# Kernel optimization log

Hardware: AMD Instinct MI355X
Metric: run time of the kernel (lower is better)

Reference implementation:

```python
import jax, jax.numpy as jnp
import numpy as np

B, N, E = 8, 10000, 320000   # graphs per batch, nodes per graph, edges per graph
C_IN, C_OUT = 128, 128
WEIGHT_STDDEV = 0.01


def setup_inputs() -> dict:
    key = jax.random.key(0)
    k_x, k_r, k_c, k_v, k_w = jax.random.split(key, 5)
    x = jax.random.normal(k_x, (B, N, C_IN), dtype=jnp.float32)
    rows = jax.random.randint(k_r, (B, E), 0, N, dtype=jnp.int32)
    cols = jax.random.randint(k_c, (B, E), 0, N, dtype=jnp.int32)
    vals = jax.random.uniform(k_v, (B, E), dtype=jnp.float32)
    W = WEIGHT_STDDEV * jax.random.normal(k_w, (C_IN, C_OUT), dtype=jnp.float32)
    b = jnp.zeros((C_OUT,), dtype=jnp.float32)  # bias_constant = 0.0
    return {"x": x, "rows": rows, "cols": cols, "vals": vals, "W": W, "b": b}


def reference(x, rows, cols, vals, W, b):
    # Per-graph sparse adjacency matmul: (A_i @ x_i), A_i in COO form.
    def spmm(r, c, v, xi):
        # gather source node features, weight by edge value, scatter-add to dst rows
        msg = v[:, None] * xi[c]                      # [E, C_IN]
        return jax.ops.segment_sum(msg, r, num_segments=N)  # [N, C_IN]

    ax = jax.vmap(spmm)(rows, cols, vals, x)          # [B, N, C_IN]
    out = jnp.einsum('bnc,co->bno', ax, W) + b        # dense transform + bias
    return jax.nn.relu(out)
```

## Files before the change

kernel.cpp:

```cpp
#include <hip/hip_runtime.h>

constexpr int BGRAPHS = 8;
constexpr int NNODES  = 10000;
constexpr int NEDGES  = 320000;
constexpr int CH      = 128;
constexpr int TOTROWS = BGRAPHS * NNODES;
constexpr int TOTEDGE = BGRAPHS * NEDGES;

constexpr int BROWS  = 32;
constexpr int BPG    = (NNODES + BROWS - 1) / BROWS;
constexpr int TOTB   = BPG * BGRAPHS;
constexpr int CHUNK  = 4000;
constexpr int NCHUNK = TOTEDGE / CHUNK;
constexpr int CAPB   = 1536;

constexpr int XROWS  = 64;
constexpr int XBPG   = (NNODES + XROWS - 1) / XROWS;
constexpr int XGRID  = 8 * XBPG;
constexpr int WTLD   = 136;

using bf16x8 = __attribute__((ext_vector_type(8))) short;
using f32x4  = __attribute__((ext_vector_type(4))) float;

__device__ __forceinline__ unsigned pack_bf16(float a, float b) {
    unsigned ua = __float_as_uint(a);
    unsigned ub = __float_as_uint(b);
    ua = (ua + 0x7FFFu + ((ua >> 16) & 1u)) >> 16;
    ub = (ub + 0x7FFFu + ((ub >> 16) & 1u)) >> 16;
    return ua | (ub << 16);
}
__device__ __forceinline__ ushort bf16_1(float f) {
    unsigned u = __float_as_uint(f);
    u = (u + 0x7FFFu + ((u >> 16) & 1u)) >> 16;
    return (ushort)u;
}

__device__ __forceinline__ unsigned pack_edge(int row5, int gcol, float v) {
    int q = __float2int_rz(v * 1024.0f);
    q = min(q, 1023);
    return ((unsigned)row5 << 27) | ((unsigned)gcol << 10) | (unsigned)q;
}

__global__ __launch_bounds__(256) void zero_int_kernel(int* __restrict__ p, int n) {
    int i = blockIdx.x * blockDim.x + threadIdx.x;
    if (i < n) p[i] = 0;
}

__global__ __launch_bounds__(256) void zero_f4_kernel(float* __restrict__ p, int n4) {
    int i = blockIdx.x * blockDim.x + threadIdx.x;
    int stride = gridDim.x * blockDim.x;
    float4 z = make_float4(0.f, 0.f, 0.f, 0.f);
    for (int j = i; j < n4; j += stride) reinterpret_cast<float4*>(p)[j] = z;
}

constexpr int SMEM_BYTES = 37120;

__global__ __launch_bounds__(256, 4) void prep_kernel(
    const int* __restrict__ rows, const int* __restrict__ cols,
    const float* __restrict__ vals, int* __restrict__ cursor,
    unsigned* __restrict__ edata,
    const float* __restrict__ x, const float* __restrict__ W,
    ushort* __restrict__ xwb) {
    __shared__ __align__(16) char smem[SMEM_BYTES];
    const int tid = threadIdx.x;

    if (blockIdx.x < NCHUNK) {
        unsigned* srec   = reinterpret_cast<unsigned*>(smem);
        unsigned* sdst   = reinterpret_cast<unsigned*>(smem + 16000);
        int*      h      = reinterpret_cast<int*>(smem + 32000);
        int*      lstart = reinterpret_cast<int*>(smem + 33280);
        int*      sbase  = reinterpret_cast<int*>(smem + 34560);
        int*      scur   = reinterpret_cast<int*>(smem + 35840);

        for (int k = tid; k < BPG; k += 256) h[k] = 0;
        __syncthreads();
        const int g  = blockIdx.x & 7;
        const int c  = blockIdx.x >> 3;
        const int e0 = g * NEDGES + c * CHUNK;
        for (int j = e0 + 4 * tid; j < e0 + CHUNK; j += 1024) {
            int4 r4 = *reinterpret_cast<const int4*>(&rows[j]);
            atomicAdd(&h[r4.x >> 5], 1);
            atomicAdd(&h[r4.y >> 5], 1);
            atomicAdd(&h[r4.z >> 5], 1);
            atomicAdd(&h[r4.w >> 5], 1);
        }
        __syncthreads();
        if (tid < 64) {
            const int b0 = tid * 5;
            int v[5];
            int s = 0;
            #pragma unroll
            for (int t = 0; t < 5; ++t) {
                int b = b0 + t;
                v[t] = (b < BPG) ? h[b] : 0;
                s += v[t];
            }
            int inc = s;
            #pragma unroll
            for (int off = 1; off < 64; off <<= 1) {
                int u = __shfl_up(inc, off);
                if (tid >= off) inc += u;
            }
            int excl = inc - s;
            #pragma unroll
            for (int t = 0; t < 5; ++t) {
                int b = b0 + t;
                if (b < BPG) { lstart[b] = excl; excl += v[t]; }
            }
        } else {
            for (int k = tid - 64; k < BPG; k += 192) {
                scur[k] = 0;
                sbase[k] = h[k] ? atomicAdd(&cursor[g * BPG + k], h[k]) : 0;
            }
        }
        __syncthreads();
        const int gbase = g * NNODES;
        for (int j = e0 + 4 * tid; j < e0 + CHUNK; j += 1024) {
            int4   r4 = *reinterpret_cast<const int4*>(&rows[j]);
            int4   c4 = *reinterpret_cast<const int4*>(&cols[j]);
            float4 v4 = *reinterpret_cast<const float4*>(&vals[j]);
            {
                int k = r4.x >> 5;
                int r = atomicAdd(&scur[k], 1);
                int pos = lstart[k] + r;
                int off = sbase[k] + r;
                srec[pos] = pack_edge(r4.x & 31, gbase + c4.x, v4.x);
                sdst[pos] = (off < CAPB) ? (unsigned)(k * CAPB + off) : 0xFFFFFFFFu;
            }
            {
                int k = r4.y >> 5;
                int r = atomicAdd(&scur[k], 1);
                int pos = lstart[k] + r;
                int off = sbase[k] + r;
                srec[pos] = pack_edge(r4.y & 31, gbase + c4.y, v4.y);
                sdst[pos] = (off < CAPB) ? (unsigned)(k * CAPB + off) : 0xFFFFFFFFu;
            }
            {
                int k = r4.z >> 5;
                int r = atomicAdd(&scur[k], 1);
                int pos = lstart[k] + r;
                int off = sbase[k] + r;
                srec[pos] = pack_edge(r4.z & 31, gbase + c4.z, v4.z);
                sdst[pos] = (off < CAPB) ? (unsigned)(k * CAPB + off) : 0xFFFFFFFFu;
            }
            {
                int k = r4.w >> 5;
                int r = atomicAdd(&scur[k], 1);
                int pos = lstart[k] + r;
                int off = sbase[k] + r;
                srec[pos] = pack_edge(r4.w & 31, gbase + c4.w, v4.w);
                sdst[pos] = (off < CAPB) ? (unsigned)(k * CAPB + off) : 0xFFFFFFFFu;
            }
        }
        __syncthreads();
        const size_t gb = (size_t)g * BPG * CAPB;
        for (int i = tid; i < CHUNK; i += 256) {
            unsigned d = sdst[i];
            if (d != 0xFFFFFFFFu) edata[gb + d] = srec[i];
        }
    } else {
        ushort* Wt = reinterpret_cast<ushort*>(smem);

        const int b2  = blockIdx.x - NCHUNK;
        const int g   = b2 & 7;
        const int rb  = b2 >> 3;
        const int row0 = rb * XROWS;
        const int rows_ib = min(XROWS, NNODES - row0);

        const float4* W4 = reinterpret_cast<const float4*>(W);
        for (int i = tid; i < 4096; i += 256) {
            float4 wv = W4[i];
            int k = i >> 5;
            int n = (i & 31) * 4;
            Wt[(n    ) * WTLD + k] = bf16_1(wv.x);
            Wt[(n + 1) * WTLD + k] = bf16_1(wv.y);
            Wt[(n + 2) * WTLD + k] = bf16_1(wv.z);
            Wt[(n + 3) * WTLD + k] = bf16_1(wv.w);
        }
        __syncthreads();

        const int w    = tid >> 6;
        const int lane = tid & 63;
        const int m16  = lane & 15;
        const int G    = lane >> 4;

        const int rA = min(row0 + w * 16 + m16, NNODES - 1);
        const float* xrow = x + ((size_t)g * NNODES + rA) * CH;

        f32x4 acc[8];
        #pragma unroll
        for (int nt = 0; nt < 8; ++nt) acc[nt] = (f32x4){0.f, 0.f, 0.f, 0.f};

        #pragma unroll
        for (int kt = 0; kt < 4; ++kt) {
            const int k0 = kt * 32 + G * 8;
            const float4* ap = reinterpret_cast<const float4*>(xrow + k0);
            float4 p = ap[0];
            float4 q = ap[1];
            union { bf16x8 vec; unsigned u[4]; } af;
            af.u[0] = pack_bf16(p.x, p.y);
            af.u[1] = pack_bf16(p.z, p.w);
            af.u[2] = pack_bf16(q.x, q.y);
            af.u[3] = pack_bf16(q.z, q.w);
            const bf16x8 avec = af.vec;
            #pragma unroll
            for (int nt = 0; nt < 8; ++nt) {
                const bf16x8 bvec = *reinterpret_cast<const bf16x8*>(
                    &Wt[(nt * 16 + m16) * WTLD + k0]);
                acc[nt] = __builtin_amdgcn_mfma_f32_16x16x32_bf16(avec, bvec,
                                                                  acc[nt], 0, 0, 0);
            }
        }

        ushort* og = xwb + ((size_t)g * NNODES + row0) * CH;
        #pragma unroll
        for (int nt = 0; nt < 8; ++nt) {
            const int col = nt * 16 + m16;
            #pragma unroll
            for (int reg = 0; reg < 4; ++reg) {
                const int rloc = w * 16 + G * 4 + reg;
                if (rloc < rows_ib)
                    og[(size_t)rloc * CH + col] = bf16_1(acc[nt][reg]);
            }
        }
    }
}

__global__ __launch_bounds__(512) void bucket_gather_kernel(
    const ushort* __restrict__ xwb, const int* __restrict__ cursor,
    const unsigned* __restrict__ edata, const float* __restrict__ bias,
    float* __restrict__ out) {
    __shared__ unsigned sorted[CAPB];
    __shared__ int cnt[BROWS];
    __shared__ int rstart[BROWS + 1];
    __shared__ int cur[BROWS];

    const int g = blockIdx.x & 7;
    const int k = blockIdx.x >> 3;
    const int bid = g * BPG + k;
    const int tid = threadIdx.x;
    const int w = tid >> 6;
    const int lane = tid & 63;
    const int eh = lane >> 5;
    const int c4 = lane & 31;
    const int rows_ib = min(BROWS, NNODES - k * BROWS);

    const size_t base = (size_t)bid * CAPB;
    const int total = min(cursor[bid], CAPB);

    unsigned e0, e1, e2;
    const bool h0 = tid < total, h1 = tid + 512 < total, h2 = tid + 1024 < total;
    if (h0) e0 = edata[base + tid];
    if (h1) e1 = edata[base + tid + 512];
    if (h2) e2 = edata[base + tid + 1024];

    if (tid < BROWS) cnt[tid] = 0;
    __syncthreads();
    if (h0) atomicAdd(&cnt[e0 >> 27], 1);
    if (h1) atomicAdd(&cnt[e1 >> 27], 1);
    if (h2) atomicAdd(&cnt[e2 >> 27], 1);
    __syncthreads();
    if (w == 0) {
        int v = (lane < BROWS) ? cnt[lane] : 0;
        int s = v;
        #pragma unroll
        for (int off = 1; off < BROWS; off <<= 1) {
            int u = __shfl_up(s, off);
            if (lane >= off) s += u;
        }
        if (lane < BROWS) { rstart[lane + 1] = s; cur[lane] = s - v; }
        if (lane == 0) rstart[0] = 0;
    }
    __syncthreads();
    if (h0) { int p = atomicAdd(&cur[e0 >> 27], 1); sorted[p] = e0; }
    if (h1) { int p = atomicAdd(&cur[e1 >> 27], 1); sorted[p] = e1; }
    if (h2) { int p = atomicAdd(&cur[e2 >> 27], 1); sorted[p] = e2; }
    __syncthreads();

    const char* xwbB = reinterpret_cast<const char*>(xwb);
    const int coff = 8 * c4;

    #define DECODE_V(M) fmaf((float)((M) & 1023u), 1.0f/1024.0f, 1.0f/2048.0f)
    #define DECODE_A(M) (((M) >> 2) & 0x01FFFF00u)

    float4 acc[4];
    #pragma unroll
    for (int i = 0; i < 4; ++i) {
        acc[i] = make_float4(0.f, 0.f, 0.f, 0.f);
        const int row = w + 8 * i;
        if (row < rows_ib) {
            int j    = rstart[row];
            int jend = rstart[row + 1];
            float4 aA = acc[i];
            float4 aB = make_float4(0.f, 0.f, 0.f, 0.f);
            for (; j + 7 < jend; j += 8) {
                unsigned m0 = sorted[j     + eh];
                unsigned m1 = sorted[j + 2 + eh];
                unsigned m2 = sorted[j + 4 + eh];
                unsigned m3 = sorted[j + 6 + eh];
                uint2 u0 = *reinterpret_cast<const uint2*>(xwbB + (DECODE_A(m0) + coff));
                uint2 u1 = *reinterpret_cast<const uint2*>(xwbB + (DECODE_A(m1) + coff));
                uint2 u2 = *reinterpret_cast<const uint2*>(xwbB + (DECODE_A(m2) + coff));
                uint2 u3 = *reinterpret_cast<const uint2*>(xwbB + (DECODE_A(m3) + coff));
                float v0 = DECODE_V(m0);
                float v1 = DECODE_V(m1);
                float v2 = DECODE_V(m2);
                float v3 = DECODE_V(m3);
                aA.x += v0 * __uint_as_float(u0.x << 16);
                aA.y += v0 * __uint_as_float(u0.x & 0xFFFF0000u);
                aA.z += v0 * __uint_as_float(u0.y << 16);
                aA.w += v0 * __uint_as_float(u0.y & 0xFFFF0000u);
                aB.x += v1 * __uint_as_float(u1.x << 16);
                aB.y += v1 * __uint_as_float(u1.x & 0xFFFF0000u);
                aB.z += v1 * __uint_as_float(u1.y << 16);
                aB.w += v1 * __uint_as_float(u1.y & 0xFFFF0000u);
                aA.x += v2 * __uint_as_float(u2.x << 16);
                aA.y += v2 * __uint_as_float(u2.x & 0xFFFF0000u);
                aA.z += v2 * __uint_as_float(u2.y << 16);
                aA.w += v2 * __uint_as_float(u2.y & 0xFFFF0000u);
                aB.x += v3 * __uint_as_float(u3.x << 16);
                aB.y += v3 * __uint_as_float(u3.x & 0xFFFF0000u);
                aB.z += v3 * __uint_as_float(u3.y << 16);
                aB.w += v3 * __uint_as_float(u3.y & 0xFFFF0000u);
            }
            for (; j + 1 < jend; j += 2) {
                unsigned m = sorted[j + eh];
                uint2 u = *reinterpret_cast<const uint2*>(xwbB + (DECODE_A(m) + coff));
                float v = DECODE_V(m);
                aA.x += v * __uint_as_float(u.x << 16);
                aA.y += v * __uint_as_float(u.x & 0xFFFF0000u);
                aA.z += v * __uint_as_float(u.y << 16);
                aA.w += v * __uint_as_float(u.y & 0xFFFF0000u);
            }
            if (j < jend && eh == 0) {
                unsigned m = sorted[j];
                uint2 u = *reinterpret_cast<const uint2*>(xwbB + (DECODE_A(m) + coff));
                float v = DECODE_V(m);
                aA.x += v * __uint_as_float(u.x << 16);
                aA.y += v * __uint_as_float(u.x & 0xFFFF0000u);
                aA.z += v * __uint_as_float(u.y << 16);
                aA.w += v * __uint_as_float(u.y & 0xFFFF0000u);
            }
            acc[i] = make_float4(aA.x + aB.x, aA.y + aB.y,
                                 aA.z + aB.z, aA.w + aB.w);
        }
    }

    const float4 b4 = *reinterpret_cast<const float4*>(&bias[4 * c4]);
    #pragma unroll
    for (int i = 0; i < 4; ++i) {
        const int row = w + 8 * i;
        if (row < rows_ib) {
            float4 a = acc[i];
            a.x += __shfl_down(a.x, 32);
            a.y += __shfl_down(a.y, 32);
            a.z += __shfl_down(a.z, 32);
            a.w += __shfl_down(a.w, 32);
            if (eh == 0) {
                a.x = fmaxf(a.x + b4.x, 0.f);
                a.y = fmaxf(a.y + b4.y, 0.f);
                a.z = fmaxf(a.z + b4.z, 0.f);
                a.w = fmaxf(a.w + b4.w, 0.f);
                *reinterpret_cast<float4*>(
                    &out[((size_t)g * NNODES + (size_t)k * BROWS + row) * CH + 4 * c4]) = a;
            }
        }
    }
}

__global__ __launch_bounds__(256) void transform_kernel(
    float* __restrict__ io, const float* __restrict__ W,
    const float* __restrict__ bias, int totalRows) {
    __shared__ float Ws[CH * CH];
    __shared__ float rbuf[8][CH];
    for (int i = threadIdx.x * 4; i < CH * CH; i += blockDim.x * 4) {
        *reinterpret_cast<float4*>(&Ws[i]) =
            *reinterpret_cast<const float4*>(&W[i]);
    }
    const int rs = threadIdx.x >> 5;
    const int o4 = threadIdx.x & 31;
    const float4 bias4 = *reinterpret_cast<const float4*>(&bias[4 * o4]);
    __syncthreads();
    for (int base = blockIdx.x * 8; base < totalRows; base += gridDim.x * 8) {
        const int row = base + rs;
        *reinterpret_cast<float4*>(&rbuf[rs][4 * o4]) =
            *reinterpret_cast<const float4*>(&io[(size_t)row * CH + 4 * o4]);
        __syncthreads();
        float4 acc = bias4;
        #pragma unroll 8
        for (int c = 0; c < CH; ++c) {
            const float rv = rbuf[rs][c];
            const float4 w4 =
                *reinterpret_cast<const float4*>(&Ws[c * CH + 4 * o4]);
            acc.x += rv * w4.x;
            acc.y += rv * w4.y;
            acc.z += rv * w4.z;
            acc.w += rv * w4.w;
        }
        acc.x = fmaxf(acc.x, 0.f);
        acc.y = fmaxf(acc.y, 0.f);
        acc.z = fmaxf(acc.z, 0.f);
        acc.w = fmaxf(acc.w, 0.f);
        *reinterpret_cast<float4*>(&io[(size_t)row * CH + 4 * o4]) = acc;
        __syncthreads();
    }
}

__global__ __launch_bounds__(256) void scatter_kernel(
    const float* __restrict__ x, const int* __restrict__ rows,
    const int* __restrict__ cols, const float* __restrict__ vals,
    float* __restrict__ ax) {
    const int lane = threadIdx.x & 63;
    int wid = (blockIdx.x * blockDim.x + threadIdx.x) >> 6;
    const int nw = (gridDim.x * blockDim.x) >> 6;
    for (int e = wid; e < TOTEDGE; e += nw) {
        int b = e / NEDGES;
        int r = rows[e];
        int c = cols[e];
        float v = vals[e];
        const float2 m =
            reinterpret_cast<const float2*>(x + (size_t)(b * NNODES + c) * CH)[lane];
        float* dst = ax + (size_t)(b * NNODES + r) * CH + 2 * lane;
        atomicAdd(dst,     v * m.x);
        atomicAdd(dst + 1, v * m.y);
    }
}

extern "C" void kernel_launch(void* const* d_in, const int* in_sizes, int n_in,
                              void* d_out, int out_size, void* d_ws, size_t ws_size,
                              hipStream_t stream) {
    const float* x    = (const float*)d_in[0];
    const int*   rows = (const int*)  d_in[1];
    const int*   cols = (const int*)  d_in[2];
    const float* vals = (const float*)d_in[3];
    const float* W    = (const float*)d_in[4];
    const float* bias = (const float*)d_in[5];
    float* out = (float*)d_out;

    const size_t off_cur   = 0;
    const size_t off_edata = (off_cur + (size_t)TOTB * 4 + 15) & ~(size_t)15;
    const size_t off_xwb   = (off_edata + (size_t)TOTB * CAPB * 4 + 15) & ~(size_t)15;
    const size_t need      = off_xwb + (size_t)TOTROWS * CH * 2;

    if (ws_size >= need) {
        int*      cursor = (int*)     ((char*)d_ws + off_cur);
        unsigned* edata  = (unsigned*)((char*)d_ws + off_edata);
        ushort*   xwb    = (ushort*)  ((char*)d_ws + off_xwb);

        zero_int_kernel<<<(TOTB + 255) / 256, 256, 0, stream>>>(cursor, TOTB);
        prep_kernel<<<NCHUNK + XGRID, 256, 0, stream>>>(rows, cols, vals,
                                                        cursor, edata, x, W, xwb);
        bucket_gather_kernel<<<TOTB, 512, 0, stream>>>(xwb, cursor, edata,
                                                       bias, out);
    } else {
        zero_f4_kernel<<<2048, 256, 0, stream>>>(out, out_size / 4);
        scatter_kernel<<<20480, 256, 0, stream>>>(x, rows, cols, vals, out);
        transform_kernel<<<2048, 256, 0, stream>>>(out, W, bias, TOTROWS);
    }
}
```

Before: 95.35 us.

## Widen bf16 gathers to 16-byte loads with four edges per wave

The bucket gather kernel now assigns 16 lanes per edge, each loading 8 bf16 channels as a uint4, so a wave processes four edges at once instead of two. Partial sums are then combined with two shuffle-reduction steps. Separately, the prep kernel's edge chunk size is halved, which doubles the number of sort blocks and shrinks their shared memory. The aim is fewer, wider gather instructions and more parallelism during prep, at the cost of more accumulator registers and more cursor atomics per bucket.

```diff
diff --git a/kernel.cpp b/kernel.cpp
--- a/kernel.cpp
+++ b/kernel.cpp
@@ -10,7 +10,7 @@
 constexpr int BROWS  = 32;
 constexpr int BPG    = (NNODES + BROWS - 1) / BROWS;
 constexpr int TOTB   = BPG * BGRAPHS;
-constexpr int CHUNK  = 4000;
+constexpr int CHUNK  = 2000;
 constexpr int NCHUNK = TOTEDGE / CHUNK;
 constexpr int CAPB   = 1536;
 
@@ -53,7 +53,7 @@
     for (int j = i; j < n4; j += stride) reinterpret_cast<float4*>(p)[j] = z;
 }
 
-constexpr int SMEM_BYTES = 37120;
+constexpr int SMEM_BYTES = 34816;
 
 __global__ __launch_bounds__(256, 4) void prep_kernel(
     const int* __restrict__ rows, const int* __restrict__ cols,
@@ -66,11 +66,11 @@
 
     if (blockIdx.x < NCHUNK) {
         unsigned* srec   = reinterpret_cast<unsigned*>(smem);
-        unsigned* sdst   = reinterpret_cast<unsigned*>(smem + 16000);
-        int*      h      = reinterpret_cast<int*>(smem + 32000);
-        int*      lstart = reinterpret_cast<int*>(smem + 33280);
-        int*      sbase  = reinterpret_cast<int*>(smem + 34560);
-        int*      scur   = reinterpret_cast<int*>(smem + 35840);
+        unsigned* sdst   = reinterpret_cast<unsigned*>(smem + 8000);
+        int*      h      = reinterpret_cast<int*>(smem + 16000);
+        int*      lstart = reinterpret_cast<int*>(smem + 17280);
+        int*      sbase  = reinterpret_cast<int*>(smem + 18560);
+        int*      scur   = reinterpret_cast<int*>(smem + 19840);
 
         for (int k = tid; k < BPG; k += 256) h[k] = 0;
         __syncthreads();
@@ -241,8 +241,8 @@
     const int tid = threadIdx.x;
     const int w = tid >> 6;
     const int lane = tid & 63;
-    const int eh = lane >> 5;
-    const int c4 = lane & 31;
+    const int eq  = lane >> 4;
+    const int ch8 = lane & 15;
     const int rows_ib = min(BROWS, NNODES - k * BROWS);
 
     const size_t base = (size_t)bid * CAPB;
@@ -278,91 +278,84 @@
     __syncthreads();
 
     const char* xwbB = reinterpret_cast<const char*>(xwb);
-    const int coff = 8 * c4;
+    const int coff = 16 * ch8;
 
     #define DECODE_V(M) fmaf((float)((M) & 1023u), 1.0f/1024.0f, 1.0f/2048.0f)
     #define DECODE_A(M) (((M) >> 2) & 0x01FFFF00u)
-
-    float4 acc[4];
+    #define ACC8(AL, AH, V, U) { \
+        AL.x += (V) * __uint_as_float((U).x << 16); \
+        AL.y += (V) * __uint_as_float((U).x & 0xFFFF0000u); \
+        AL.z += (V) * __uint_as_float((U).y << 16); \
+        AL.w += (V) * __uint_as_float((U).y & 0xFFFF0000u); \
+        AH.x += (V) * __uint_as_float((U).z << 16); \
+        AH.y += (V) * __uint_as_float((U).z & 0xFFFF0000u); \
+        AH.z += (V) * __uint_as_float((U).w << 16); \
+        AH.w += (V) * __uint_as_float((U).w & 0xFFFF0000u); }
+
+    float4 accL[4], accH[4];
     #pragma unroll
     for (int i = 0; i < 4; ++i) {
-        acc[i] = make_float4(0.f, 0.f, 0.f, 0.f);
+        accL[i] = make_float4(0.f, 0.f, 0.f, 0.f);
+        accH[i] = make_float4(0.f, 0.f, 0.f, 0.f);
         const int row = w + 8 * i;
         if (row < rows_ib) {
             int j    = rstart[row];
             int jend = rstart[row + 1];
-            float4 aA = acc[i];
-            float4 aB = make_float4(0.f, 0.f, 0.f, 0.f);
+            float4 bL = make_float4(0.f, 0.f, 0.f, 0.f), bH = bL;
             for (; j + 7 < jend; j += 8) {
-                unsigned m0 = sorted[j     + eh];
-                unsigned m1 = sorted[j + 2 + eh];
-                unsigned m2 = sorted[j + 4 + eh];
-                unsigned m3 = sorted[j + 6 + eh];
-                uint2 u0 = *reinterpret_cast<const uint2*>(xwbB + (DECODE_A(m0) + coff));
-                uint2 u1 = *reinterpret_cast<const uint2*>(xwbB + (DECODE_A(m1) + coff));
-                uint2 u2 = *reinterpret_cast<const uint2*>(xwbB + (DECODE_A(m2) + coff));
-                uint2 u3 = *reinterpret_cast<const uint2*>(xwbB + (DECODE_A(m3) + coff));
+                unsigned m0 = sorted[j     + eq];
+                unsigned m1 = sorted[j + 4 + eq];
+                uint4 u0 = *reinterpret_cast<const uint4*>(xwbB + (DECODE_A(m0) + coff));
+                uint4 u1 = *reinterpret_cast<const uint4*>(xwbB + (DECODE_A(m1) + coff));
                 float v0 = DECODE_V(m0);
                 float v1 = DECODE_V(m1);
-                float v2 = DECODE_V(m2);
-                float v3 = DECODE_V(m3);
-                aA.x += v0 * __uint_as_float(u0.x << 16);
-                aA.y += v0 * __uint_as_float(u0.x & 0xFFFF0000u);
-                aA.z += v0 * __uint_as_float(u0.y << 16);
-                aA.w += v0 * __uint_as_float(u0.y & 0xFFFF0000u);
-                aB.x += v1 * __uint_as_float(u1.x << 16);
-                aB.y += v1 * __uint_as_float(u1.x & 0xFFFF0000u);
-                aB.z += v1 * __uint_as_float(u1.y << 16);
-                aB.w += v1 * __uint_as_float(u1.y & 0xFFFF0000u);
-                aA.x += v2 * __uint_as_float(u2.x << 16);
-                aA.y += v2 * __uint_as_float(u2.x & 0xFFFF0000u);
-                aA.z += v2 * __uint_as_float(u2.y << 16);
-                aA.w += v2 * __uint_as_float(u2.y & 0xFFFF0000u);
-                aB.x += v3 * __uint_as_float(u3.x << 16);
-                aB.y += v3 * __uint_as_float(u3.x & 0xFFFF0000u);
-                aB.z += v3 * __uint_as_float(u3.y << 16);
-                aB.w += v3 * __uint_as_float(u3.y & 0xFFFF0000u);
-            }
-            for (; j + 1 < jend; j += 2) {
-                unsigned m = sorted[j + eh];
-                uint2 u = *reinterpret_cast<const uint2*>(xwbB + (DECODE_A(m) + coff));
+                ACC8(accL[i], accH[i], v0, u0)
+                ACC8(bL, bH, v1, u1)
+            }
+            if (j + eq < jend) {
+                unsigned m = sorted[j + eq];
+                uint4 u = *reinterpret_cast<const uint4*>(xwbB + (DECODE_A(m) + coff));
                 float v = DECODE_V(m);
-                aA.x += v * __uint_as_float(u.x << 16);
-                aA.y += v * __uint_as_float(u.x & 0xFFFF0000u);
-                aA.z += v * __uint_as_float(u.y << 16);
-                aA.w += v * __uint_as_float(u.y & 0xFFFF0000u);
-            }
-            if (j < jend && eh == 0) {
-                unsigned m = sorted[j];
-                uint2 u = *reinterpret_cast<const uint2*>(xwbB + (DECODE_A(m) + coff));
+                ACC8(accL[i], accH[i], v, u)
+            }
+            if (j + 4 + eq < jend) {
+                unsigned m = sorted[j + 4 + eq];
+                uint4 u = *reinterpret_cast<const uint4*>(xwbB + (DECODE_A(m) + coff));
                 float v = DECODE_V(m);
-                aA.x += v * __uint_as_float(u.x << 16);
-                aA.y += v * __uint_as_float(u.x & 0xFFFF0000u);
-                aA.z += v * __uint_as_float(u.y << 16);
-                aA.w += v * __uint_as_float(u.y & 0xFFFF0000u);
-            }
-            acc[i] = make_float4(aA.x + aB.x, aA.y + aB.y,
-                                 aA.z + aB.z, aA.w + aB.w);
-        }
-    }
-
-    const float4 b4 = *reinterpret_cast<const float4*>(&bias[4 * c4]);
+                ACC8(bL, bH, v, u)
+            }
+            accL[i].x += bL.x; accL[i].y += bL.y; accL[i].z += bL.z; accL[i].w += bL.w;
+            accH[i].x += bH.x; accH[i].y += bH.y; accH[i].z += bH.z; accH[i].w += bH.w;
+        }
+    }
+
+    const float4 bLo = *reinterpret_cast<const float4*>(&bias[8 * ch8]);
+    const float4 bHi = *reinterpret_cast<const float4*>(&bias[8 * ch8 + 4]);
     #pragma unroll
     for (int i = 0; i < 4; ++i) {
         const int row = w + 8 * i;
         if (row < rows_ib) {
-            float4 a = acc[i];
-            a.x += __shfl_down(a.x, 32);
-            a.y += __shfl_down(a.y, 32);
-            a.z += __shfl_down(a.z, 32);
-            a.w += __shfl_down(a.w, 32);
-            if (eh == 0) {
-                a.x = fmaxf(a.x + b4.x, 0.f);
-                a.y = fmaxf(a.y + b4.y, 0.f);
-                a.z = fmaxf(a.z + b4.z, 0.f);
-                a.w = fmaxf(a.w + b4.w, 0.f);
-                *reinterpret_cast<float4*>(
-                    &out[((size_t)g * NNODES + (size_t)k * BROWS + row) * CH + 4 * c4]) = a;
+            float4 aL = accL[i], aH = accH[i];
+            aL.x += __shfl_down(aL.x, 16); aL.y += __shfl_down(aL.y, 16);
+            aL.z += __shfl_down(aL.z, 16); aL.w += __shfl_down(aL.w, 16);
+            aH.x += __shfl_down(aH.x, 16); aH.y += __shfl_down(aH.y, 16);
+            aH.z += __shfl_down(aH.z, 16); aH.w += __shfl_down(aH.w, 16);
+            aL.x += __shfl_down(aL.x, 32); aL.y += __shfl_down(aL.y, 32);
+            aL.z += __shfl_down(aL.z, 32); aL.w += __shfl_down(aL.w, 32);
+            aH.x += __shfl_down(aH.x, 32); aH.y += __shfl_down(aH.y, 32);
+            aH.z += __shfl_down(aH.z, 32); aH.w += __shfl_down(aH.w, 32);
+            if (eq == 0) {
+                aL.x = fmaxf(aL.x + bLo.x, 0.f);
+                aL.y = fmaxf(aL.y + bLo.y, 0.f);
+                aL.z = fmaxf(aL.z + bLo.z, 0.f);
+                aL.w = fmaxf(aL.w + bLo.w, 0.f);
+                aH.x = fmaxf(aH.x + bHi.x, 0.f);
+                aH.y = fmaxf(aH.y + bHi.y, 0.f);
+                aH.z = fmaxf(aH.z + bHi.z, 0.f);
+                aH.w = fmaxf(aH.w + bHi.w, 0.f);
+                float* orow = &out[((size_t)g * NNODES + (size_t)k * BROWS + row) * CH + 8 * ch8];
+                *reinterpret_cast<float4*>(orow)     = aL;
+                *reinterpret_cast<float4*>(orow + 4) = aH;
             }
         }
     }
```

Measured after the change: 98.37 us. 3.2% more time.
